# Performance work log

Hardware: AMD Instinct MI355X
Metric: run time of the kernel (lower is better)

The kernel has to match this reference:

```python
import jax, jax.numpy as jnp
import numpy as np

N_NODES = 50000
N_EDGES = 600000
D_IN, D_H1, D_H2 = 128, 128, 64


def setup_inputs() -> dict:
    key = jax.random.key(0)
    ks = jax.random.split(key, 8)
    x = jax.random.normal(ks[0], (N_NODES, D_IN), dtype=jnp.float32)
    edge_index = jax.random.randint(ks[1], (2, N_EDGES), 0, N_NODES, dtype=jnp.int64)
    # Glorot-style init for GCN weights, uniform for biases
    W1 = jax.random.normal(ks[2], (D_IN, D_H1), dtype=jnp.float32) / np.sqrt(D_IN)
    b1 = jnp.zeros((D_H1,), dtype=jnp.float32)
    W2 = jax.random.normal(ks[3], (D_H1, D_H2), dtype=jnp.float32) / np.sqrt(D_H1)
    b2 = jnp.zeros((D_H2,), dtype=jnp.float32)
    W3 = jax.random.normal(ks[4], (D_H2, 1), dtype=jnp.float32) / np.sqrt(D_H2)
    b3 = jnp.zeros((1,), dtype=jnp.float32)
    return {"x": x, "edge_index": edge_index, "W1": W1, "b1": b1,
            "W2": W2, "b2": b2, "W3": W3, "b3": b3}


def _gcn_norm(edge_index, n_nodes, dtype):
    # Add self-loops, then symmetric normalization deg^-1/2 * deg^-1/2 (PyG gcn_norm).
    loop = jnp.arange(n_nodes, dtype=edge_index.dtype)
    src = jnp.concatenate([edge_index[0], loop])
    dst = jnp.concatenate([edge_index[1], loop])
    deg = jax.ops.segment_sum(jnp.ones_like(dst, dtype=dtype), dst, num_segments=n_nodes)
    dinv = jnp.where(deg > 0, jax.lax.rsqrt(deg), 0.0)
    norm = dinv[src] * dinv[dst]  # [E+N]
    return src, dst, norm


def _gcn_conv(x, src, dst, norm, W, b, n_nodes):
    h = x @ W                       # [N, F_out]
    msg = h[src] * norm[:, None]    # gather + scale: [E+N, F_out]
    out = jax.ops.segment_sum(msg, dst, num_segments=n_nodes)  # scatter-add
    return out + b


def reference(x, edge_index, W1, b1, W2, b2, W3, b3):
    n = x.shape[0]
    src, dst, norm = _gcn_norm(edge_index, n, x.dtype)
    h = jax.nn.relu(_gcn_conv(x, src, dst, norm, W1, b1, n))
    # dropout is identity in eval mode
    h = jax.nn.relu(_gcn_conv(h, src, dst, norm, W2, b2, n))
    return h @ W3 + b3  # [N, 1]
```

## Files before the change

### kernel.cpp

```cpp
#include <hip/hip_runtime.h>

#define N_NODES 50000
#define N_EDGES 600000
#define SCAN_BLOCKS ((N_NODES + 1023) / 1024)
#define CNT_BLOCKS ((N_EDGES + 255) / 256)

typedef unsigned int u32;
typedef unsigned short u16;
typedef __attribute__((ext_vector_type(8))) short short8;
typedef __attribute__((ext_vector_type(4))) float f32x4;

__device__ __forceinline__ u16 f2bf(float f) {
    u32 u = __float_as_uint(f);
    u32 r = (u + 0x7fffu + ((u >> 16) & 1u)) >> 16;
    return (u16)r;
}
__device__ __forceinline__ float bf_lo(u32 u) { return __uint_as_float(u << 16); }
__device__ __forceinline__ float bf_hi(u32 u) { return __uint_as_float(u & 0xffff0000u); }


__global__ void count_prep(const int* __restrict__ ei, int* __restrict__ deg,
                           int* __restrict__ rank,
                           const float* __restrict__ W1, const float* __restrict__ W2,
                           u16* __restrict__ W1t, u16* __restrict__ W2t) {
    int b = blockIdx.x;
    if (b < CNT_BLOCKS) {
        int e = b * 256 + threadIdx.x;
        if (e < N_EDGES) {
            int d = ei[N_EDGES + e];
            rank[e] = atomicAdd(&deg[d], 1);
        }
    } else {
        int i = (b - CNT_BLOCKS) * 256 + threadIdx.x;
        if (i < 128 * 128) {
            int n = i >> 7, k = i & 127;
            W1t[i] = f2bf(W1[k * 128 + n]);
        } else {
            int j = i - 128 * 128;
            int n = j >> 7, k = j & 127;
            W2t[j] = f2bf(W2[k * 64 + n]);
        }
    }
}

__global__ __launch_bounds__(1024) void scan_blocks_k(const int* __restrict__ deg,
                                                      int* __restrict__ rs,
                                                      int* __restrict__ partials,
                                                      float* __restrict__ dinv) {
    __shared__ int wsum[16];
    int i = blockIdx.x * 1024 + threadIdx.x;
    int v = (i < N_NODES) ? deg[i] : 0;
    if (i < N_NODES) dinv[i] = rsqrtf((float)(v + 1));
    int lane = threadIdx.x & 63, w = threadIdx.x >> 6;
    int s = v;
#pragma unroll
    for (int off = 1; off < 64; off <<= 1) {
        int t = __shfl_up(s, off, 64);
        if (lane >= off) s += t;
    }
    if (lane == 63) wsum[w] = s;
    __syncthreads();
    if (w == 0) {
        int ws = (lane < 16) ? wsum[lane] : 0;
#pragma unroll
        for (int off = 1; off < 16; off <<= 1) {
            int t = __shfl_up(ws, off, 64);
            if (lane >= off) ws += t;
        }
        if (lane < 16) wsum[lane] = ws;
    }
    __syncthreads();
    int incl = s + ((w > 0) ? wsum[w - 1] : 0);
    if (i < N_NODES) rs[i] = incl - v;
    if (threadIdx.x == 1023) partials[blockIdx.x] = incl;
}

__global__ __launch_bounds__(256) void finalize_csr(int* __restrict__ rs,
                                                    const int* __restrict__ partials) {
    __shared__ int spref;
    int b = blockIdx.x;
    if (threadIdx.x < 64) {
        int p = (threadIdx.x < SCAN_BLOCKS) ? partials[threadIdx.x] : 0;
        int orig = p;
#pragma unroll
        for (int off = 1; off < 64; off <<= 1) {
            int t = __shfl_up(p, off, 64);
            if ((threadIdx.x & 63) >= off) p += t;
        }
        if (threadIdx.x == (b >> 2)) spref = p - orig;
    }
    __syncthreads();
    int i = b * 256 + threadIdx.x;
    if (i < N_NODES) rs[i] += spref;
    if (i == 0) rs[N_NODES] = N_EDGES;
}

__global__ void fill_csr(const int* __restrict__ ei, const int* __restrict__ rs,
                         const int* __restrict__ rank, int* __restrict__ col) {
    int e = blockIdx.x * 256 + threadIdx.x;
    if (e < N_EDGES) {
        int s = ei[e];
        int d = ei[N_EDGES + e];
        col[rs[d] + rank[e]] = s;
    }
}


#define SL 136

__global__ __launch_bounds__(256) void gemm1_mfma(const float* __restrict__ A,
                                                  const u16* __restrict__ Bt,
                                                  const float* __restrict__ dinv,
                                                  u16* __restrict__ out) {
    __shared__ u16 As[64 * SL];
    __shared__ u16 Bs[128 * SL];
    const int tid = threadIdx.x;
    const int m0 = blockIdx.x * 64;
    {
        int row = tid >> 2, c0 = (tid & 3) * 32;
        bool ok = (m0 + row) < N_NODES;
        const float4* src = (const float4*)&A[(size_t)(m0 + row) * 128 + c0];
        u16* dst = &As[row * SL + c0];
#pragma unroll
        for (int i = 0; i < 8; ++i) {
            float4 v = ok ? src[i] : make_float4(0.f, 0.f, 0.f, 0.f);
            u32 lo = (u32)f2bf(v.x) | ((u32)f2bf(v.y) << 16);
            u32 hi = (u32)f2bf(v.z) | ((u32)f2bf(v.w) << 16);
            *(uint2*)&dst[i * 4] = make_uint2(lo, hi);
        }
    }
    {
        int n = tid >> 1, h = (tid & 1) * 64;
        const uint4* src = (const uint4*)&Bt[n * 128 + h];
        u16* dst = &Bs[n * SL + h];
#pragma unroll
        for (int i = 0; i < 8; ++i) *(uint4*)&dst[i * 8] = src[i];
    }
    __syncthreads();

    const int l = tid & 63, w = tid >> 6;
    const int q = l >> 4, r16 = l & 15;
    const int m_off = w * 16;
    f32x4 acc[8] = {};
#pragma unroll
    for (int kt = 0; kt < 128; kt += 32) {
        short8 a = *(const short8*)&As[(m_off + r16) * SL + kt + q * 8];
        short8 b[8];
#pragma unroll
        for (int tn = 0; tn < 8; ++tn)
            b[tn] = *(const short8*)&Bs[(tn * 16 + r16) * SL + kt + q * 8];
#pragma unroll
        for (int tn = 0; tn < 8; ++tn)
            acc[tn] = __builtin_amdgcn_mfma_f32_16x16x32_bf16(a, b[tn], acc[tn], 0, 0, 0);
    }
#pragma unroll
    for (int r = 0; r < 4; ++r) {
        int row = m0 + m_off + q * 4 + r;
        if (row < N_NODES) {
            float dv = dinv[row];
#pragma unroll
            for (int tn = 0; tn < 8; ++tn)
                out[(size_t)row * 128 + tn * 16 + r16] = f2bf(acc[tn][r] * dv);
        }
    }
}


__global__ __launch_bounds__(256) void gemm2_mfma(const u16* __restrict__ A,
                                                  const u16* __restrict__ Bt,
                                                  const float* __restrict__ dinv,
                                                  u16* __restrict__ out) {
    __shared__ u16 As[128 * SL];
    __shared__ u16 Bs[64 * SL];
    const int tid = threadIdx.x;
    const int m0 = blockIdx.x * 128;
    {
        int row = tid >> 1, h = (tid & 1) * 64;
        bool ok = (m0 + row) < N_NODES;
        const uint4* src = (const uint4*)&A[(size_t)(m0 + row) * 128 + h];
        u16* dst = &As[row * SL + h];
#pragma unroll
        for (int i = 0; i < 8; ++i) {
            uint4 v = ok ? src[i] : make_uint4(0, 0, 0, 0);
            *(uint4*)&dst[i * 8] = v;
        }
    }
    {
        int n = tid >> 2, s0 = (tid & 3) * 32;
        const uint4* src = (const uint4*)&Bt[n * 128 + s0];
        u16* dst = &Bs[n * SL + s0];
#pragma unroll
        for (int i = 0; i < 4; ++i) *(uint4*)&dst[i * 8] = src[i];
    }
    __syncthreads();

    const int l = tid & 63, w = tid >> 6;
    const int q = l >> 4, r16 = l & 15;
    const int m_base = w * 32;
    f32x4 acc[2][4] = {};
#pragma unroll
    for (int kt = 0; kt < 128; kt += 32) {
        short8 a[2];
        a[0] = *(const short8*)&As[(m_base + r16) * SL + kt + q * 8];
        a[1] = *(const short8*)&As[(m_base + 16 + r16) * SL + kt + q * 8];
        short8 b[4];
#pragma unroll
        for (int tn = 0; tn < 4; ++tn)
            b[tn] = *(const short8*)&Bs[(tn * 16 + r16) * SL + kt + q * 8];
#pragma unroll
        for (int tm = 0; tm < 2; ++tm)
#pragma unroll
            for (int tn = 0; tn < 4; ++tn)
                acc[tm][tn] =
                    __builtin_amdgcn_mfma_f32_16x16x32_bf16(a[tm], b[tn], acc[tm][tn], 0, 0, 0);
    }
#pragma unroll
    for (int tm = 0; tm < 2; ++tm)
#pragma unroll
        for (int r = 0; r < 4; ++r) {
            int row = m0 + m_base + tm * 16 + q * 4 + r;
            if (row < N_NODES) {
                float dv = dinv[row];
#pragma unroll
                for (int tn = 0; tn < 4; ++tn)
                    out[(size_t)row * 64 + tn * 16 + r16] = f2bf(acc[tm][tn][r] * dv);
            }
        }
}


__global__ __launch_bounds__(256) void agg_relu128_bf(const u16* __restrict__ hs,
                                                      const int* __restrict__ rs,
                                                      const int* __restrict__ col,
                                                      const float* __restrict__ dinv,
                                                      const float* __restrict__ bias,
                                                      u16* __restrict__ out) {
    int node = blockIdx.x * 16 + (threadIdx.x >> 4);
    int lane = threadIdx.x & 15;
    if (node >= N_NODES) return;
    const uint4* rows = (const uint4*)hs;
    float acc[8] = {};
    auto accum = [&](uint4 v) {
        acc[0] += bf_lo(v.x); acc[1] += bf_hi(v.x);
        acc[2] += bf_lo(v.y); acc[3] += bf_hi(v.y);
        acc[4] += bf_lo(v.z); acc[5] += bf_hi(v.z);
        acc[6] += bf_lo(v.w); acc[7] += bf_hi(v.w);
    };
    accum(rows[(size_t)node * 16 + lane]);
    int e = rs[node], e1 = rs[node + 1];
    for (; e + 8 <= e1; e += 8) {
        int c[8];
#pragma unroll
        for (int j = 0; j < 8; ++j) c[j] = col[e + j];
        uint4 v[8];
#pragma unroll
        for (int j = 0; j < 8; ++j) v[j] = rows[(size_t)c[j] * 16 + lane];
#pragma unroll
        for (int j = 0; j < 8; ++j) accum(v[j]);
    }
    for (; e + 4 <= e1; e += 4) {
        int c[4];
#pragma unroll
        for (int j = 0; j < 4; ++j) c[j] = col[e + j];
        uint4 v[4];
#pragma unroll
        for (int j = 0; j < 4; ++j) v[j] = rows[(size_t)c[j] * 16 + lane];
#pragma unroll
        for (int j = 0; j < 4; ++j) accum(v[j]);
    }
    for (; e < e1; ++e) accum(rows[(size_t)col[e] * 16 + lane]);
    float dv = dinv[node];
    int fo = lane * 8;
    u32 pk[4];
#pragma unroll
    for (int j = 0; j < 4; ++j) {
        u16 a = f2bf(fmaxf(fmaf(dv, acc[2 * j], bias[fo + 2 * j]), 0.f));
        u16 b = f2bf(fmaxf(fmaf(dv, acc[2 * j + 1], bias[fo + 2 * j + 1]), 0.f));
        pk[j] = (u32)a | ((u32)b << 16);
    }
    *(uint4*)&out[(size_t)node * 128 + fo] = make_uint4(pk[0], pk[1], pk[2], pk[3]);
}


__global__ __launch_bounds__(256) void agg_final_bf(const u16* __restrict__ hs,
                                                    const int* __restrict__ rs,
                                                    const int* __restrict__ col,
                                                    const float* __restrict__ dinv,
                                                    const float* __restrict__ b2,
                                                    const float* __restrict__ W3,
                                                    const float* __restrict__ b3,
                                                    float* __restrict__ out) {
    int node = blockIdx.x * 32 + (threadIdx.x >> 3);
    int lane = threadIdx.x & 7;
    if (node >= N_NODES) return;
    const uint4* rows = (const uint4*)hs;
    float acc[8] = {};
    auto accum = [&](uint4 v) {
        acc[0] += bf_lo(v.x); acc[1] += bf_hi(v.x);
        acc[2] += bf_lo(v.y); acc[3] += bf_hi(v.y);
        acc[4] += bf_lo(v.z); acc[5] += bf_hi(v.z);
        acc[6] += bf_lo(v.w); acc[7] += bf_hi(v.w);
    };
    accum(rows[(size_t)node * 8 + lane]);
    int e = rs[node], e1 = rs[node + 1];
    for (; e + 8 <= e1; e += 8) {
        int c[8];
#pragma unroll
        for (int j = 0; j < 8; ++j) c[j] = col[e + j];
        uint4 v[8];
#pragma unroll
        for (int j = 0; j < 8; ++j) v[j] = rows[(size_t)c[j] * 8 + lane];
#pragma unroll
        for (int j = 0; j < 8; ++j) accum(v[j]);
    }
    for (; e + 4 <= e1; e += 4) {
        int c[4];
#pragma unroll
        for (int j = 0; j < 4; ++j) c[j] = col[e + j];
        uint4 v[4];
#pragma unroll
        for (int j = 0; j < 4; ++j) v[j] = rows[(size_t)c[j] * 8 + lane];
#pragma unroll
        for (int j = 0; j < 4; ++j) accum(v[j]);
    }
    for (; e < e1; ++e) accum(rows[(size_t)col[e] * 8 + lane]);
    float dv = dinv[node];
    int fo = lane * 8;
    float v = 0.f;
#pragma unroll
    for (int j = 0; j < 8; ++j)
        v += fmaxf(fmaf(dv, acc[j], b2[fo + j]), 0.f) * W3[fo + j];
#pragma unroll
    for (int m = 4; m > 0; m >>= 1) v += __shfl_xor(v, m, 64);
    if (lane == 0) out[node] = v + b3[0];
}


extern "C" void kernel_launch(void* const* d_in, const int* in_sizes, int n_in,
                              void* d_out, int out_size, void* d_ws, size_t ws_size,
                              hipStream_t stream) {
    const float* x  = (const float*)d_in[0];
    const int*   ei = (const int*)d_in[1];
    const float* W1 = (const float*)d_in[2];
    const float* b1 = (const float*)d_in[3];
    const float* W2 = (const float*)d_in[4];
    const float* b2 = (const float*)d_in[5];
    const float* W3 = (const float*)d_in[6];
    const float* b3 = (const float*)d_in[7];
    float* out = (float*)d_out;

    char* ws = (char*)d_ws;
    size_t off = 0;
    auto alloc = [&](size_t bytes) -> void* {
        void* p = ws + off;
        off = (off + bytes + 255) & ~(size_t)255;
        return p;
    };
    int*   deg      = (int*)alloc(N_NODES * sizeof(int));
    int*   rs       = (int*)alloc((N_NODES + 1) * sizeof(int));
    int*   rank     = (int*)alloc(N_EDGES * sizeof(int));
    int*   partials = (int*)alloc(64 * sizeof(int));
    int*   col      = (int*)alloc(N_EDGES * sizeof(int));
    float* dinv     = (float*)alloc(N_NODES * sizeof(float));
    u16*   W1t      = (u16*)alloc(128 * 128 * sizeof(u16));
    u16*   W2t      = (u16*)alloc(64 * 128 * sizeof(u16));
    u16*   hs1      = (u16*)alloc((size_t)N_NODES * 128 * sizeof(u16));
    u16*   t1       = (u16*)alloc((size_t)N_NODES * 128 * sizeof(u16));
    u16*   hs2      = (u16*)alloc((size_t)N_NODES * 64 * sizeof(u16));

    hipMemsetAsync(deg, 0, N_NODES * sizeof(int), stream);
    count_prep<<<CNT_BLOCKS + 96, 256, 0, stream>>>(ei, deg, rank, W1, W2, W1t, W2t);
    scan_blocks_k<<<SCAN_BLOCKS, 1024, 0, stream>>>(deg, rs, partials, dinv);
    finalize_csr<<<(N_NODES + 255) / 256, 256, 0, stream>>>(rs, partials);
    fill_csr<<<(N_EDGES + 255) / 256, 256, 0, stream>>>(ei, rs, rank, col);

    gemm1_mfma<<<(N_NODES + 63) / 64, 256, 0, stream>>>(x, W1t, dinv, hs1);
    agg_relu128_bf<<<(N_NODES + 15) / 16, 256, 0, stream>>>(hs1, rs, col, dinv, b1, t1);
    gemm2_mfma<<<(N_NODES + 127) / 128, 256, 0, stream>>>(t1, W2t, dinv, hs2);
    agg_final_bf<<<(N_NODES + 31) / 32, 256, 0, stream>>>(hs2, rs, col, dinv, b2, W3, b3, out);
}
```

Before: 188.7 us.

## Fuse CSR fill into GEMM1, aggregation into GEMM2, drop finalize pass

```diff
diff --git a/kernel.cpp b/kernel.cpp
--- a/kernel.cpp
+++ b/kernel.cpp
@@ -4,6 +4,8 @@
 #define N_EDGES 600000
 #define SCAN_BLOCKS ((N_NODES + 1023) / 1024)
 #define CNT_BLOCKS ((N_EDGES + 255) / 256)
+#define GB1 ((N_NODES + 63) / 64)
+#define FB  ((N_EDGES + 255) / 256)
 
 typedef unsigned int u32;
 typedef unsigned short u16;
@@ -17,6 +19,21 @@
 }
 __device__ __forceinline__ float bf_lo(u32 u) { return __uint_as_float(u << 16); }
 __device__ __forceinline__ float bf_hi(u32 u) { return __uint_as_float(u & 0xffff0000u); }
+
+__device__ __forceinline__ void load_pref(const int* __restrict__ partials, int* pref) {
+    if (threadIdx.x < 64) {
+        int t = threadIdx.x;
+        int p = (t < SCAN_BLOCKS) ? partials[t] : 0;
+        int orig = p;
+#pragma unroll
+        for (int off = 1; off < 64; off <<= 1) {
+            int q = __shfl_up(p, off, 64);
+            if (t >= off) p += q;
+        }
+        if (t < SCAN_BLOCKS) pref[t] = p - orig;
+    }
+    __syncthreads();
+}
 
 
 __global__ void count_prep(const int* __restrict__ ei, int* __restrict__ deg,
@@ -72,50 +89,38 @@
     __syncthreads();
     int incl = s + ((w > 0) ? wsum[w - 1] : 0);
     if (i < N_NODES) rs[i] = incl - v;
+    if (i == N_NODES - 1) rs[N_NODES] = incl;
     if (threadIdx.x == 1023) partials[blockIdx.x] = incl;
 }
 
-__global__ __launch_bounds__(256) void finalize_csr(int* __restrict__ rs,
-                                                    const int* __restrict__ partials) {
-    __shared__ int spref;
-    int b = blockIdx.x;
-    if (threadIdx.x < 64) {
-        int p = (threadIdx.x < SCAN_BLOCKS) ? partials[threadIdx.x] : 0;
-        int orig = p;
-#pragma unroll
-        for (int off = 1; off < 64; off <<= 1) {
-            int t = __shfl_up(p, off, 64);
-            if ((threadIdx.x & 63) >= off) p += t;
-        }
-        if (threadIdx.x == (b >> 2)) spref = p - orig;
-    }
-    __syncthreads();
-    int i = b * 256 + threadIdx.x;
-    if (i < N_NODES) rs[i] += spref;
-    if (i == 0) rs[N_NODES] = N_EDGES;
-}
-
-__global__ void fill_csr(const int* __restrict__ ei, const int* __restrict__ rs,
-                         const int* __restrict__ rank, int* __restrict__ col) {
-    int e = blockIdx.x * 256 + threadIdx.x;
-    if (e < N_EDGES) {
-        int s = ei[e];
-        int d = ei[N_EDGES + e];
-        col[rs[d] + rank[e]] = s;
-    }
-}
-
 
 #define SL 136
 
-__global__ __launch_bounds__(256) void gemm1_mfma(const float* __restrict__ A,
+__global__ __launch_bounds__(256) void gemm1_fill(const float* __restrict__ A,
                                                   const u16* __restrict__ Bt,
                                                   const float* __restrict__ dinv,
-                                                  u16* __restrict__ out) {
+                                                  u16* __restrict__ out,
+                                                  const int* __restrict__ ei,
+                                                  const int* __restrict__ rs,
+                                                  const int* __restrict__ rank,
+                                                  const int* __restrict__ partials,
+                                                  int* __restrict__ col) {
     __shared__ u16 As[64 * SL];
     __shared__ u16 Bs[128 * SL];
+    __shared__ int pref[64];
     const int tid = threadIdx.x;
-    const int m0 = blockIdx.x * 64;
+    const int b = blockIdx.x;
+    if (b >= GB1) {
+        load_pref(partials, pref);
+        int e = (b - GB1) * 256 + tid;
+        if (e < N_EDGES) {
+            int s = ei[e];
+            int d = ei[N_EDGES + e];
+            col[rs[d] + pref[d >> 10] + rank[e]] = s;
+        }
+        return;
+    }
+    const int m0 = b * 64;
     {
         int row = tid >> 2, c0 = (tid & 3) * 32;
         bool ok = (m0 + row) < N_NODES;
@@ -145,13 +150,13 @@
 #pragma unroll
     for (int kt = 0; kt < 128; kt += 32) {
         short8 a = *(const short8*)&As[(m_off + r16) * SL + kt + q * 8];
-        short8 b[8];
+        short8 bb[8];
 #pragma unroll
         for (int tn = 0; tn < 8; ++tn)
-            b[tn] = *(const short8*)&Bs[(tn * 16 + r16) * SL + kt + q * 8];
+            bb[tn] = *(const short8*)&Bs[(tn * 16 + r16) * SL + kt + q * 8];
 #pragma unroll
         for (int tn = 0; tn < 8; ++tn)
-            acc[tn] = __builtin_amdgcn_mfma_f32_16x16x32_bf16(a, b[tn], acc[tn], 0, 0, 0);
+            acc[tn] = __builtin_amdgcn_mfma_f32_16x16x32_bf16(a, bb[tn], acc[tn], 0, 0, 0);
     }
 #pragma unroll
     for (int r = 0; r < 4; ++r) {
@@ -166,25 +171,19 @@
 }
 
 
-__global__ __launch_bounds__(256) void gemm2_mfma(const u16* __restrict__ A,
-                                                  const u16* __restrict__ Bt,
-                                                  const float* __restrict__ dinv,
-                                                  u16* __restrict__ out) {
-    __shared__ u16 As[128 * SL];
+__global__ __launch_bounds__(256) void agg_gemm2(const u16* __restrict__ hs,
+                                                 const int* __restrict__ rs,
+                                                 const int* __restrict__ partials,
+                                                 const int* __restrict__ col,
+                                                 const float* __restrict__ dinv,
+                                                 const float* __restrict__ bias,
+                                                 const u16* __restrict__ Bt,
+                                                 u16* __restrict__ out) {
+    __shared__ u16 As[64 * SL];
     __shared__ u16 Bs[64 * SL];
+    __shared__ int pref[64];
     const int tid = threadIdx.x;
-    const int m0 = blockIdx.x * 128;
-    {
-        int row = tid >> 1, h = (tid & 1) * 64;
-        bool ok = (m0 + row) < N_NODES;
-        const uint4* src = (const uint4*)&A[(size_t)(m0 + row) * 128 + h];
-        u16* dst = &As[row * SL + h];
-#pragma unroll
-        for (int i = 0; i < 8; ++i) {
-            uint4 v = ok ? src[i] : make_uint4(0, 0, 0, 0);
-            *(uint4*)&dst[i * 8] = v;
-        }
-    }
+    const int m0 = blockIdx.x * 64;
     {
         int n = tid >> 2, s0 = (tid & 3) * 32;
         const uint4* src = (const uint4*)&Bt[n * 128 + s0];
@@ -192,104 +191,101 @@
 #pragma unroll
         for (int i = 0; i < 4; ++i) *(uint4*)&dst[i * 8] = src[i];
     }
+    load_pref(partials, pref);
+
+    const uint4* rows = (const uint4*)hs;
+    const int lane = tid & 15;
+    const int fo = lane * 8;
+#pragma unroll
+    for (int p = 0; p < 4; ++p) {
+        int nl = p * 16 + (tid >> 4);
+        int node = m0 + nl;
+        uint4 pk = make_uint4(0, 0, 0, 0);
+        if (node < N_NODES) {
+            float acc[8] = {};
+            auto accum = [&](uint4 v) {
+                acc[0] += bf_lo(v.x); acc[1] += bf_hi(v.x);
+                acc[2] += bf_lo(v.y); acc[3] += bf_hi(v.y);
+                acc[4] += bf_lo(v.z); acc[5] += bf_hi(v.z);
+                acc[6] += bf_lo(v.w); acc[7] += bf_hi(v.w);
+            };
+            accum(rows[(size_t)node * 16 + lane]);
+            int e = rs[node] + pref[node >> 10];
+            int e1 = rs[node + 1] + pref[(node + 1) >> 10];
+            for (; e + 8 <= e1; e += 8) {
+                int c[8];
+#pragma unroll
+                for (int j = 0; j < 8; ++j) c[j] = col[e + j];
+                uint4 v[8];
+#pragma unroll
+                for (int j = 0; j < 8; ++j) v[j] = rows[(size_t)c[j] * 16 + lane];
+#pragma unroll
+                for (int j = 0; j < 8; ++j) accum(v[j]);
+            }
+            for (; e + 4 <= e1; e += 4) {
+                int c[4];
+#pragma unroll
+                for (int j = 0; j < 4; ++j) c[j] = col[e + j];
+                uint4 v[4];
+#pragma unroll
+                for (int j = 0; j < 4; ++j) v[j] = rows[(size_t)c[j] * 16 + lane];
+#pragma unroll
+                for (int j = 0; j < 4; ++j) accum(v[j]);
+            }
+            for (; e < e1; ++e) accum(rows[(size_t)col[e] * 16 + lane]);
+            float dv = dinv[node];
+            u32 w0[4];
+#pragma unroll
+            for (int j = 0; j < 4; ++j) {
+                u16 a = f2bf(fmaxf(fmaf(dv, acc[2 * j], bias[fo + 2 * j]), 0.f));
+                u16 b = f2bf(fmaxf(fmaf(dv, acc[2 * j + 1], bias[fo + 2 * j + 1]), 0.f));
+                w0[j] = (u32)a | ((u32)b << 16);
+            }
+            pk = make_uint4(w0[0], w0[1], w0[2], w0[3]);
+        }
+        *(uint4*)&As[nl * SL + fo] = pk;
+    }
     __syncthreads();
 
     const int l = tid & 63, w = tid >> 6;
     const int q = l >> 4, r16 = l & 15;
-    const int m_base = w * 32;
-    f32x4 acc[2][4] = {};
+    const int m_off = w * 16;
+    f32x4 acc[4] = {};
 #pragma unroll
     for (int kt = 0; kt < 128; kt += 32) {
-        short8 a[2];
-        a[0] = *(const short8*)&As[(m_base + r16) * SL + kt + q * 8];
-        a[1] = *(const short8*)&As[(m_base + 16 + r16) * SL + kt + q * 8];
-        short8 b[4];
+        short8 a = *(const short8*)&As[(m_off + r16) * SL + kt + q * 8];
+        short8 bb[4];
 #pragma unroll
         for (int tn = 0; tn < 4; ++tn)
-            b[tn] = *(const short8*)&Bs[(tn * 16 + r16) * SL + kt + q * 8];
-#pragma unroll
-        for (int tm = 0; tm < 2; ++tm)
+            bb[tn] = *(const short8*)&Bs[(tn * 16 + r16) * SL + kt + q * 8];
+#pragma unroll
+        for (int tn = 0; tn < 4; ++tn)
+            acc[tn] = __builtin_amdgcn_mfma_f32_16x16x32_bf16(a, bb[tn], acc[tn], 0, 0, 0);
+    }
+#pragma unroll
+    for (int r = 0; r < 4; ++r) {
+        int row = m0 + m_off + q * 4 + r;
+        if (row < N_NODES) {
+            float dv = dinv[row];
 #pragma unroll
             for (int tn = 0; tn < 4; ++tn)
-                acc[tm][tn] =
-                    __builtin_amdgcn_mfma_f32_16x16x32_bf16(a[tm], b[tn], acc[tm][tn], 0, 0, 0);
-    }
-#pragma unroll
-    for (int tm = 0; tm < 2; ++tm)
-#pragma unroll
-        for (int r = 0; r < 4; ++r) {
-            int row = m0 + m_base + tm * 16 + q * 4 + r;
-            if (row < N_NODES) {
-                float dv = dinv[row];
-#pragma unroll
-                for (int tn = 0; tn < 4; ++tn)
-                    out[(size_t)row * 64 + tn * 16 + r16] = f2bf(acc[tm][tn][r] * dv);
-            }
-        }
-}
-
-
-__global__ __launch_bounds__(256) void agg_relu128_bf(const u16* __restrict__ hs,
-                                                      const int* __restrict__ rs,
-                                                      const int* __restrict__ col,
-                                                      const float* __restrict__ dinv,
-                                                      const float* __restrict__ bias,
-                                                      u16* __restrict__ out) {
-    int node = blockIdx.x * 16 + (threadIdx.x >> 4);
-    int lane = threadIdx.x & 15;
-    if (node >= N_NODES) return;
-    const uint4* rows = (const uint4*)hs;
-    float acc[8] = {};
-    auto accum = [&](uint4 v) {
-        acc[0] += bf_lo(v.x); acc[1] += bf_hi(v.x);
-        acc[2] += bf_lo(v.y); acc[3] += bf_hi(v.y);
-        acc[4] += bf_lo(v.z); acc[5] += bf_hi(v.z);
-        acc[6] += bf_lo(v.w); acc[7] += bf_hi(v.w);
-    };
-    accum(rows[(size_t)node * 16 + lane]);
-    int e = rs[node], e1 = rs[node + 1];
-    for (; e + 8 <= e1; e += 8) {
-        int c[8];
-#pragma unroll
-        for (int j = 0; j < 8; ++j) c[j] = col[e + j];
-        uint4 v[8];
-#pragma unroll
-        for (int j = 0; j < 8; ++j) v[j] = rows[(size_t)c[j] * 16 + lane];
-#pragma unroll
-        for (int j = 0; j < 8; ++j) accum(v[j]);
-    }
-    for (; e + 4 <= e1; e += 4) {
-        int c[4];
-#pragma unroll
-        for (int j = 0; j < 4; ++j) c[j] = col[e + j];
-        uint4 v[4];
-#pragma unroll
-        for (int j = 0; j < 4; ++j) v[j] = rows[(size_t)c[j] * 16 + lane];
-#pragma unroll
-        for (int j = 0; j < 4; ++j) accum(v[j]);
-    }
-    for (; e < e1; ++e) accum(rows[(size_t)col[e] * 16 + lane]);
-    float dv = dinv[node];
-    int fo = lane * 8;
-    u32 pk[4];
-#pragma unroll
-    for (int j = 0; j < 4; ++j) {
-        u16 a = f2bf(fmaxf(fmaf(dv, acc[2 * j], bias[fo + 2 * j]), 0.f));
-        u16 b = f2bf(fmaxf(fmaf(dv, acc[2 * j + 1], bias[fo + 2 * j + 1]), 0.f));
-        pk[j] = (u32)a | ((u32)b << 16);
-    }
-    *(uint4*)&out[(size_t)node * 128 + fo] = make_uint4(pk[0], pk[1], pk[2], pk[3]);
+                out[(size_t)row * 64 + tn * 16 + r16] = f2bf(acc[tn][r] * dv);
+        }
+    }
 }
 
 
 __global__ __launch_bounds__(256) void agg_final_bf(const u16* __restrict__ hs,
                                                     const int* __restrict__ rs,
+                                                    const int* __restrict__ partials,
                                                     const int* __restrict__ col,
                                                     const float* __restrict__ dinv,
                                                     const float* __restrict__ b2,
                                                     const float* __restrict__ W3,
                                                     const float* __restrict__ b3,
                                                     float* __restrict__ out) {
+    __shared__ int pref[64];
+    load_pref(partials, pref);
     int node = blockIdx.x * 32 + (threadIdx.x >> 3);
     int lane = threadIdx.x & 7;
     if (node >= N_NODES) return;
@@ -302,7 +298,8 @@
         acc[6] += bf_lo(v.w); acc[7] += bf_hi(v.w);
     };
     accum(rows[(size_t)node * 8 + lane]);
-    int e = rs[node], e1 = rs[node + 1];
+    int e = rs[node] + pref[node >> 10];
+    int e1 = rs[node + 1] + pref[(node + 1) >> 10];
     for (; e + 8 <= e1; e += 8) {
         int c[8];
 #pragma unroll
@@ -365,17 +362,14 @@
     u16*   W1t      = (u16*)alloc(128 * 128 * sizeof(u16));
     u16*   W2t      = (u16*)alloc(64 * 128 * sizeof(u16));
     u16*   hs1      = (u16*)alloc((size_t)N_NODES * 128 * sizeof(u16));
-    u16*   t1       = (u16*)alloc((size_t)N_NODES * 128 * sizeof(u16));
     u16*   hs2      = (u16*)alloc((size_t)N_NODES * 64 * sizeof(u16));
 
     hipMemsetAsync(deg, 0, N_NODES * sizeof(int), stream);
     count_prep<<<CNT_BLOCKS + 96, 256, 0, stream>>>(ei, deg, rank, W1, W2, W1t, W2t);
     scan_blocks_k<<<SCAN_BLOCKS, 1024, 0, stream>>>(deg, rs, partials, dinv);
-    finalize_csr<<<(N_NODES + 255) / 256, 256, 0, stream>>>(rs, partials);
-    fill_csr<<<(N_EDGES + 255) / 256, 256, 0, stream>>>(ei, rs, rank, col);
-
-    gemm1_mfma<<<(N_NODES + 63) / 64, 256, 0, stream>>>(x, W1t, dinv, hs1);
-    agg_relu128_bf<<<(N_NODES + 15) / 16, 256, 0, stream>>>(hs1, rs, col, dinv, b1, t1);
-    gemm2_mfma<<<(N_NODES + 127) / 128, 256, 0, stream>>>(t1, W2t, dinv, hs2);
-    agg_final_bf<<<(N_NODES + 31) / 32, 256, 0, stream>>>(hs2, rs, col, dinv, b2, W3, b3, out);
-}
+    gemm1_fill<<<GB1 + FB, 256, 0, stream>>>(x, W1t, dinv, hs1, ei, rs, rank, partials, col);
+    agg_gemm2<<<(N_NODES + 63) / 64, 256, 0, stream>>>(hs1, rs, partials, col, dinv, b1,
+                                                       W2t, hs2);
+    agg_final_bf<<<(N_NODES + 31) / 32, 256, 0, stream>>>(hs2, rs, partials, col, dinv,
+                                                          b2, W3, b3, out);
+}
```

New measurement: 178.9 us. 1.05x faster.
